# Performance work log

Hardware: AMD Instinct MI355X
Metric: run time of the kernel (lower is better)

The kernel has to match this reference:

```python
import jax, jax.numpy as jnp
import numpy as np

B, S, D_MODEL, H = 4, 2048, 1024, 16
D_K = D_MODEL // H


def setup_inputs() -> dict:
    key = jax.random.key(0)
    kx, kq, kk, kv, ko = jax.random.split(key, 5)
    scale = 1.0 / np.sqrt(D_MODEL)
    return {
        "x": jax.random.normal(kx, (B, S, D_MODEL), dtype=jnp.float32),
        "W_q": jax.random.normal(kq, (D_MODEL, D_MODEL), dtype=jnp.float32) * scale,
        "W_k": jax.random.normal(kk, (D_MODEL, D_MODEL), dtype=jnp.float32) * scale,
        "W_v": jax.random.normal(kv, (D_MODEL, D_MODEL), dtype=jnp.float32) * scale,
        "W_out": jax.random.normal(ko, (D_MODEL, D_MODEL), dtype=jnp.float32) * scale,
    }


def reference(x, W_q, W_k, W_v, W_out):
    # nn.Linear(bias=False): y = x @ W.T; weights stored as (out, in).
    Bx, Sx, D = x.shape
    q = (x @ W_q.T).reshape(Bx, Sx, H, D_K).transpose(0, 2, 1, 3)  # (B,H,S,d_k)
    k = (x @ W_k.T).reshape(Bx, Sx, H, D_K).transpose(0, 2, 1, 3)
    v = (x @ W_v.T).reshape(Bx, Sx, H, D_K).transpose(0, 2, 1, 3)
    scores = jnp.einsum("bhsd,bhtd->bhst", q, k) / jnp.sqrt(jnp.float32(D_K))
    attn = jax.nn.softmax(scores, axis=-1)
    out = jnp.einsum("bhst,bhtd->bhsd", attn, v)  # (B,H,S,d_k)
    out = out.transpose(0, 2, 1, 3).reshape(Bx, Sx, D)  # combine heads
    return out @ W_out.T
```

## Files before the change

### kernel.cpp

```cpp
#include <hip/hip_runtime.h>

#define BATCH 4
#define SEQ 2048
#define DM 1024
#define NH 16
#define DK 64

typedef unsigned short u16;
typedef unsigned int u32;
typedef __attribute__((ext_vector_type(8))) short bfrag;
typedef __attribute__((ext_vector_type(4))) float ffrag;

__device__ inline u16 f2bf(float f) {
  union { float f; u32 u; } v; v.f = f;
  u32 u = v.u;
  return (u16)((u + 0x7FFFu + ((u >> 16) & 1u)) >> 16);
}
__device__ inline float bf2f(u16 u) {
  union { u32 u; float f; } v; v.u = ((u32)u) << 16;
  return v.f;
}
__device__ inline ffrag MFMA(bfrag a, bfrag b, ffrag c) {
  return __builtin_amdgcn_mfma_f32_16x16x32_bf16(a, b, c, 0, 0, 0);
}

__device__ __forceinline__ void g2l16(const u16* g, u16* l) {
  __builtin_amdgcn_global_load_lds(
      (const __attribute__((address_space(1))) u16*)g,
      (__attribute__((address_space(3))) u16*)l, 16, 0, 0);
}

__global__ __launch_bounds__(256) void cvt_all(
    const float* __restrict__ x,
    const float* __restrict__ a, const float* __restrict__ b,
    const float* __restrict__ c, const float* __restrict__ d,
    u16* __restrict__ ox,
    u16* __restrict__ oa, u16* __restrict__ ob,
    u16* __restrict__ oc, u16* __restrict__ od) {
  int blk = blockIdx.x;
  const float* in;
  u16* out;
  int i;
  if (blk < 8192) {
    in = x; out = ox; i = blk * 256 + threadIdx.x;
  } else {
    int wb = blk - 8192;
    int which = wb >> 10;
    in = which == 0 ? a : which == 1 ? b : which == 2 ? c : d;
    out = which == 0 ? oa : which == 1 ? ob : which == 2 ? oc : od;
    i = (wb & 1023) * 256 + threadIdx.x;
  }
  float4 v = ((const float4*)in)[i];
  union { u16 u[4]; uint2 dd; } o;
  o.u[0] = f2bf(v.x); o.u[1] = f2bf(v.y); o.u[2] = f2bf(v.z); o.u[3] = f2bf(v.w);
  ((uint2*)out)[i] = o.dd;
}

__global__ __launch_bounds__(256) void gemm_qkv(
    const u16* __restrict__ xb,
    const u16* __restrict__ Wq, const u16* __restrict__ Wk,
    const u16* __restrict__ Wv,
    u16* __restrict__ Qb, u16* __restrict__ Ksw, u16* __restrict__ Vsw) {
  const int bid = blockIdx.x;
  const int xcd = bid & 7, s8 = bid >> 3;
  const int ym = (xcd << 3) | (s8 & 7);
  const int xn = (s8 >> 3) & 7;
  const int z = s8 >> 6;
  const u16* Bm = z == 0 ? Wq : z == 1 ? Wk : Wv;

  const int K = DM;
  const int bm = ym * 128, bn = xn * 128;
  __shared__ __align__(16) u16 As[128 * 64];
  __shared__ __align__(16) u16 Bs[128 * 64];
  const int tid = threadIdx.x;
  const int lane = tid & 63;
  const int w = tid >> 6;
  const int wr = w >> 1, wc = w & 1;
  const int l15 = lane & 15, quad = lane >> 4;
  const int srow = tid >> 3;
  const int scol = (((tid & 7) ^ (srow & 7)) * 8);

  ffrag acc[4][4] = {};

  for (int k0 = 0; k0 < K; k0 += 64) {
    __syncthreads();
#pragma unroll
    for (int c = 0; c < 4; c++) {
      g2l16(&xb[(size_t)(bm + c * 32 + srow) * K + k0 + scol], &As[c * 2048 + tid * 8]);
      g2l16(&Bm[(size_t)(bn + c * 32 + srow) * K + k0 + scol], &Bs[c * 2048 + tid * 8]);
    }
    __syncthreads();
#pragma unroll
    for (int kk = 0; kk < 2; kk++) {
      bfrag af[4], bf[4];
      if (z == 2) {
#pragma unroll
        for (int i = 0; i < 4; i++)
          af[i] = *(const bfrag*)(&As[(wr * 64 + i * 16 + l15) * 64 +
                                      ((kk * 4 + quad) ^ (l15 & 7)) * 8]);
#pragma unroll
        for (int j = 0; j < 4; j++)
          bf[j] = *(const bfrag*)(&Bs[(wc * 64 + j * 16 + l15) * 64 +
                                      ((kk * 4 + quad) ^ (l15 & 7)) * 8]);
      } else {
#pragma unroll
        for (int i = 0; i < 4; i++)
          af[i] = *(const bfrag*)(&Bs[(wr * 64 + i * 16 + l15) * 64 +
                                      ((kk * 4 + quad) ^ (l15 & 7)) * 8]);
#pragma unroll
        for (int j = 0; j < 4; j++)
          bf[j] = *(const bfrag*)(&As[(wc * 64 + j * 16 + l15) * 64 +
                                      ((kk * 4 + quad) ^ (l15 & 7)) * 8]);
      }
#pragma unroll
      for (int i = 0; i < 4; i++)
#pragma unroll
        for (int j = 0; j < 4; j++)
          acc[i][j] = MFMA(af[i], bf[j], acc[i][j]);
    }
  }

  if (z == 0) {
#pragma unroll
    for (int i = 0; i < 4; i++)
#pragma unroll
      for (int j = 0; j < 4; j++) {
        int mo = bn + wr * 64 + i * 16 + quad * 4;
        int nt = bm + wc * 64 + j * 16 + l15;
        int b = nt >> 11, s = nt & 2047;
        int h = mo >> 6, d = mo & 63;
        union { u16 u[4]; uint2 dd; } o;
#pragma unroll
        for (int r = 0; r < 4; r++) o.u[r] = f2bf(acc[i][j][r]);
        *(uint2*)(&Qb[(((size_t)(b * NH + h)) * SEQ + s) * DK + d]) = o.dd;
      }
  } else if (z == 1) {
#pragma unroll
    for (int i = 0; i < 4; i++)
#pragma unroll
      for (int j = 0; j < 4; j++) {
        int mo = bn + wr * 64 + i * 16 + quad * 4;
        int nt = bm + wc * 64 + j * 16 + l15;
        int b = nt >> 11, s = nt & 2047;
        int h = mo >> 6;
        size_t hb = (size_t)(b * NH + h) * (SEQ * DK);
        size_t off = hb + (size_t)(s >> 6) * 4096 +
            (size_t)((j * 2 + (i >> 1)) * 64 +
                     ((i * 2 + (quad >> 1)) & 3) * 16 + l15) * 8 +
            (quad & 1) * 4;
        union { u16 u[4]; uint2 dd; } o;
#pragma unroll
        for (int r = 0; r < 4; r++) o.u[r] = f2bf(acc[i][j][r]);
        *(uint2*)(&Ksw[off]) = o.dd;
      }
  } else {
#pragma unroll
    for (int i = 0; i < 4; i++)
#pragma unroll
      for (int j = 0; j < 4; j++) {
        int mt = bm + wr * 64 + i * 16 + quad * 4;
        int no = bn + wc * 64 + j * 16 + l15;
        int b = mt >> 11, s = mt & 2047;
        int h = no >> 6;
        size_t hb = (size_t)(b * NH + h) * (SEQ * DK);
        size_t off = hb + (size_t)(s >> 6) * 4096 +
            (size_t)((j * 2 + (i >> 1)) * 64 + quad * 16 + l15) * 8 +
            (i & 1) * 4;
        union { u16 u[4]; uint2 dd; } o;
#pragma unroll
        for (int r = 0; r < 4; r++) o.u[r] = f2bf(acc[i][j][r]);
        *(uint2*)(&Vsw[off]) = o.dd;
      }
  }
}

__global__ __launch_bounds__(256) void gemm_out(
    const u16* __restrict__ Ab, const u16* __restrict__ Wo, float* __restrict__ C) {
  const int K = DM, N = DM;
  const int bid = blockIdx.x;
  const int xcd = bid & 7, s8 = bid >> 3;
  const int ym = (xcd << 3) | (s8 & 7);
  const int xn = s8 >> 3;
  const int bm = ym * 128, bn = xn * 128;
  __shared__ __align__(16) u16 As[128 * 64];
  __shared__ __align__(16) u16 Bs[128 * 64];
  const int tid = threadIdx.x;
  const int lane = tid & 63;
  const int w = tid >> 6;
  const int wr = w >> 1, wc = w & 1;
  const int l15 = lane & 15, quad = lane >> 4;
  const int srow = tid >> 3;
  const int scol = (((tid & 7) ^ (srow & 7)) * 8);

  ffrag acc[4][4] = {};

  for (int k0 = 0; k0 < K; k0 += 64) {
    __syncthreads();
#pragma unroll
    for (int c = 0; c < 4; c++) {
      g2l16(&Ab[(size_t)(bm + c * 32 + srow) * K + k0 + scol], &As[c * 2048 + tid * 8]);
      g2l16(&Wo[(size_t)(bn + c * 32 + srow) * K + k0 + scol], &Bs[c * 2048 + tid * 8]);
    }
    __syncthreads();
#pragma unroll
    for (int kk = 0; kk < 2; kk++) {
      bfrag af[4], bf[4];
#pragma unroll
      for (int i = 0; i < 4; i++)
        af[i] = *(const bfrag*)(&Bs[(wr * 64 + i * 16 + l15) * 64 +
                                    ((kk * 4 + quad) ^ (l15 & 7)) * 8]);
#pragma unroll
      for (int j = 0; j < 4; j++)
        bf[j] = *(const bfrag*)(&As[(wc * 64 + j * 16 + l15) * 64 +
                                    ((kk * 4 + quad) ^ (l15 & 7)) * 8]);
#pragma unroll
      for (int i = 0; i < 4; i++)
#pragma unroll
        for (int j = 0; j < 4; j++)
          acc[i][j] = MFMA(af[i], bf[j], acc[i][j]);
    }
  }

#pragma unroll
  for (int i = 0; i < 4; i++)
#pragma unroll
    for (int j = 0; j < 4; j++) {
      int no = bn + wr * 64 + i * 16 + quad * 4;
      int mt = bm + wc * 64 + j * 16 + l15;
      *(ffrag*)(&C[(size_t)mt * N + no]) = acc[i][j];
    }
}

__global__ __launch_bounds__(256) void attn(
    const u16* __restrict__ Qb, const u16* __restrict__ Ksw,
    const u16* __restrict__ Vsw, u16* __restrict__ Ab) {
  const int bh = blockIdx.x;
  const int b = bh >> 4, h = bh & 15;
  const int qbase = blockIdx.y * 128;
  const int tid = threadIdx.x;
  const int w = tid >> 6, lane = tid & 63;
  const int l15 = lane & 15, quad = lane >> 4;

  __shared__ __align__(16) u16 Kt[2][4096];
  __shared__ __align__(16) u16 Vt[2][4096];

  const size_t hbase = (size_t)bh * SEQ * DK;

  const float qscale = 0.125f * 1.4426950408889634f;
  bfrag q[2][2];
#pragma unroll
  for (int i = 0; i < 2; i++)
#pragma unroll
    for (int kk = 0; kk < 2; kk++) {
      bfrag t = *(const bfrag*)(&Qb[hbase +
          (size_t)(qbase + w * 32 + i * 16 + l15) * DK + kk * 32 + quad * 8]);
#pragma unroll
      for (int e = 0; e < 8; e++)
        q[i][kk][e] = (short)f2bf(bf2f((u16)t[e]) * qscale);
    }

  ffrag O[4][2] = {};
  float lsum[2] = {0.f, 0.f};

  {
    const u16* ks = &Ksw[hbase];
    const u16* vs = &Vsw[hbase];
    g2l16(&ks[tid * 8], &Kt[0][tid * 8]);
    g2l16(&ks[2048 + tid * 8], &Kt[0][2048 + tid * 8]);
    g2l16(&vs[tid * 8], &Vt[0][tid * 8]);
    g2l16(&vs[2048 + tid * 8], &Vt[0][2048 + tid * 8]);
  }

  for (int t = 0; t < SEQ / 64; t++) {
    const int buf = t & 1;
    __syncthreads();
    if (t + 1 < SEQ / 64) {
      const u16* ks = &Ksw[hbase + (size_t)(t + 1) * 4096];
      const u16* vs = &Vsw[hbase + (size_t)(t + 1) * 4096];
      g2l16(&ks[tid * 8], &Kt[buf ^ 1][tid * 8]);
      g2l16(&ks[2048 + tid * 8], &Kt[buf ^ 1][2048 + tid * 8]);
      g2l16(&vs[tid * 8], &Vt[buf ^ 1][tid * 8]);
      g2l16(&vs[2048 + tid * 8], &Vt[buf ^ 1][2048 + tid * 8]);
    }

    __builtin_amdgcn_s_setprio(1);
    u32 pb[4][2][2];
#pragma unroll
    for (int j = 0; j < 4; j++) {
      bfrag k0f = *(const bfrag*)(&Kt[buf][((j * 2 + 0) * 64 + lane) * 8]);
      bfrag k1f = *(const bfrag*)(&Kt[buf][((j * 2 + 1) * 64 + lane) * 8]);
#pragma unroll
      for (int i = 0; i < 2; i++) {
        ffrag z = {};
        z = MFMA(k0f, q[i][0], z);
        z = MFMA(k1f, q[i][1], z);
        u32 u[4]; float ts = 0.f;
#pragma unroll
        for (int r = 0; r < 4; r++) {
          float p = __builtin_amdgcn_exp2f(z[r]);
          u[r] = __float_as_uint(p);
          ts += __uint_as_float(u[r] & 0xffff0000u);
        }
        lsum[i] += ts;
        pb[j][i][0] = __builtin_amdgcn_perm(u[1], u[0], 0x07060302u);
        pb[j][i][1] = __builtin_amdgcn_perm(u[3], u[2], 0x07060302u);
      }
    }

#pragma unroll
    for (int wnd = 0; wnd < 2; wnd++) {
      union { u32 d[4]; bfrag v; } px0, px1;
      px0.d[0] = pb[2 * wnd][0][0];     px0.d[1] = pb[2 * wnd][0][1];
      px0.d[2] = pb[2 * wnd + 1][0][0]; px0.d[3] = pb[2 * wnd + 1][0][1];
      px1.d[0] = pb[2 * wnd][1][0];     px1.d[1] = pb[2 * wnd][1][1];
      px1.d[2] = pb[2 * wnd + 1][1][0]; px1.d[3] = pb[2 * wnd + 1][1][1];
#pragma unroll
      for (int db = 0; db < 4; db++) {
        bfrag vf = *(const bfrag*)(&Vt[buf][((db * 2 + wnd) * 64 + lane) * 8]);
        O[db][0] = MFMA(vf, px0.v, O[db][0]);
        O[db][1] = MFMA(vf, px1.v, O[db][1]);
      }
    }
    __builtin_amdgcn_s_setprio(0);
  }

  float rl[2];
#pragma unroll
  for (int i = 0; i < 2; i++) {
    float s = lsum[i];
    s += __shfl_xor(s, 16);
    s += __shfl_xor(s, 32);
    rl[i] = 1.0f / s;
  }

  const size_t obase = ((size_t)b * SEQ) * DM + (size_t)h * DK;
#pragma unroll
  for (int db = 0; db < 4; db++)
#pragma unroll
    for (int i = 0; i < 2; i++) {
      int s = qbase + w * 32 + i * 16 + l15;
      union { u16 u[4]; uint2 d; } o;
#pragma unroll
      for (int r = 0; r < 4; r++) o.u[r] = f2bf(O[db][i][r] * rl[i]);
      *(uint2*)(&Ab[obase + (size_t)s * DM + db * 16 + quad * 4]) = o.d;
    }
}

extern "C" void kernel_launch(void* const* d_in, const int* in_sizes, int n_in,
                              void* d_out, int out_size, void* d_ws, size_t ws_size,
                              hipStream_t stream) {
  const float* x  = (const float*)d_in[0];
  const float* Wq = (const float*)d_in[1];
  const float* Wk = (const float*)d_in[2];
  const float* Wv = (const float*)d_in[3];
  const float* Wo = (const float*)d_in[4];
  float* out = (float*)d_out;

  char* ws = (char*)d_ws;
  u16* xb  = (u16*)(ws + 0);
  u16* Wqb = (u16*)(ws + 16777216);
  u16* Wkb = (u16*)(ws + 18874368);
  u16* Wvb = (u16*)(ws + 20971520);
  u16* Wob = (u16*)(ws + 23068672);
  u16* Qb  = (u16*)(ws + 25165824);
  u16* Ksw = (u16*)(ws + 41943040);
  u16* Vsw = (u16*)(ws + 58720256);
  u16* Ab  = (u16*)(ws + 75497472);
  const size_t NEED = 92274688;
  if (ws_size < NEED) return;

  cvt_all<<<12288, 256, 0, stream>>>(x, Wq, Wk, Wv, Wo, xb, Wqb, Wkb, Wvb, Wob);

  gemm_qkv<<<1536, 256, 0, stream>>>(xb, Wqb, Wkb, Wvb, Qb, Ksw, Vsw);

  dim3 gat(BATCH * NH, SEQ / 128);
  attn<<<gat, 256, 0, stream>>>(Qb, Ksw, Vsw, Ab);

  gemm_out<<<512, 256, 0, stream>>>(Ab, Wob, out);
}
```

Baseline: 268.5 us.

## Double-buffer LDS tiles in QKV and output GEMMs with K-tile 32

```diff
diff --git a/kernel.cpp b/kernel.cpp
--- a/kernel.cpp
+++ b/kernel.cpp
@@ -70,54 +70,55 @@
 
   const int K = DM;
   const int bm = ym * 128, bn = xn * 128;
-  __shared__ __align__(16) u16 As[128 * 64];
-  __shared__ __align__(16) u16 Bs[128 * 64];
+  __shared__ __align__(16) u16 As[2][128 * 32];
+  __shared__ __align__(16) u16 Bs[2][128 * 32];
   const int tid = threadIdx.x;
   const int lane = tid & 63;
   const int w = tid >> 6;
   const int wr = w >> 1, wc = w & 1;
   const int l15 = lane & 15, quad = lane >> 4;
-  const int srow = tid >> 3;
-  const int scol = (((tid & 7) ^ (srow & 7)) * 8);
+  const int srow = tid >> 2;
+  const int scol = (((tid & 3) ^ ((tid >> 3) & 3)) * 8);
+  const int sq = (quad ^ ((l15 >> 1) & 3)) * 8;
 
   ffrag acc[4][4] = {};
 
-  for (int k0 = 0; k0 < K; k0 += 64) {
+  g2l16(&xb[(size_t)(bm + srow) * K + scol], &As[0][tid * 8]);
+  g2l16(&xb[(size_t)(bm + 64 + srow) * K + scol], &As[0][(tid + 256) * 8]);
+  g2l16(&Bm[(size_t)(bn + srow) * K + scol], &Bs[0][tid * 8]);
+  g2l16(&Bm[(size_t)(bn + 64 + srow) * K + scol], &Bs[0][(tid + 256) * 8]);
+
+  for (int kt = 0; kt < K / 32; ++kt) {
+    const int buf = kt & 1;
     __syncthreads();
-#pragma unroll
-    for (int c = 0; c < 4; c++) {
-      g2l16(&xb[(size_t)(bm + c * 32 + srow) * K + k0 + scol], &As[c * 2048 + tid * 8]);
-      g2l16(&Bm[(size_t)(bn + c * 32 + srow) * K + k0 + scol], &Bs[c * 2048 + tid * 8]);
-    }
-    __syncthreads();
-#pragma unroll
-    for (int kk = 0; kk < 2; kk++) {
-      bfrag af[4], bf[4];
-      if (z == 2) {
-#pragma unroll
-        for (int i = 0; i < 4; i++)
-          af[i] = *(const bfrag*)(&As[(wr * 64 + i * 16 + l15) * 64 +
-                                      ((kk * 4 + quad) ^ (l15 & 7)) * 8]);
-#pragma unroll
-        for (int j = 0; j < 4; j++)
-          bf[j] = *(const bfrag*)(&Bs[(wc * 64 + j * 16 + l15) * 64 +
-                                      ((kk * 4 + quad) ^ (l15 & 7)) * 8]);
-      } else {
-#pragma unroll
-        for (int i = 0; i < 4; i++)
-          af[i] = *(const bfrag*)(&Bs[(wr * 64 + i * 16 + l15) * 64 +
-                                      ((kk * 4 + quad) ^ (l15 & 7)) * 8]);
-#pragma unroll
-        for (int j = 0; j < 4; j++)
-          bf[j] = *(const bfrag*)(&As[(wc * 64 + j * 16 + l15) * 64 +
-                                      ((kk * 4 + quad) ^ (l15 & 7)) * 8]);
-      }
+    if (kt + 1 < K / 32) {
+      const int k1 = (kt + 1) * 32;
+      g2l16(&xb[(size_t)(bm + srow) * K + k1 + scol], &As[buf ^ 1][tid * 8]);
+      g2l16(&xb[(size_t)(bm + 64 + srow) * K + k1 + scol], &As[buf ^ 1][(tid + 256) * 8]);
+      g2l16(&Bm[(size_t)(bn + srow) * K + k1 + scol], &Bs[buf ^ 1][tid * 8]);
+      g2l16(&Bm[(size_t)(bn + 64 + srow) * K + k1 + scol], &Bs[buf ^ 1][(tid + 256) * 8]);
+    }
+    bfrag af[4], bf[4];
+    if (z == 2) {
 #pragma unroll
       for (int i = 0; i < 4; i++)
-#pragma unroll
-        for (int j = 0; j < 4; j++)
-          acc[i][j] = MFMA(af[i], bf[j], acc[i][j]);
-    }
+        af[i] = *(const bfrag*)(&As[buf][(wr * 64 + i * 16 + l15) * 32 + sq]);
+#pragma unroll
+      for (int j = 0; j < 4; j++)
+        bf[j] = *(const bfrag*)(&Bs[buf][(wc * 64 + j * 16 + l15) * 32 + sq]);
+    } else {
+#pragma unroll
+      for (int i = 0; i < 4; i++)
+        af[i] = *(const bfrag*)(&Bs[buf][(wr * 64 + i * 16 + l15) * 32 + sq]);
+#pragma unroll
+      for (int j = 0; j < 4; j++)
+        bf[j] = *(const bfrag*)(&As[buf][(wc * 64 + j * 16 + l15) * 32 + sq]);
+    }
+#pragma unroll
+    for (int i = 0; i < 4; i++)
+#pragma unroll
+      for (int j = 0; j < 4; j++)
+        acc[i][j] = MFMA(af[i], bf[j], acc[i][j]);
   }
 
   if (z == 0) {
@@ -139,8 +140,8 @@
     for (int i = 0; i < 4; i++)
 #pragma unroll
       for (int j = 0; j < 4; j++) {
+        int nt = bm + wc * 64 + j * 16 + l15;
         int mo = bn + wr * 64 + i * 16 + quad * 4;
-        int nt = bm + wc * 64 + j * 16 + l15;
         int b = nt >> 11, s = nt & 2047;
         int h = mo >> 6;
         size_t hb = (size_t)(b * NH + h) * (SEQ * DK);
@@ -182,43 +183,46 @@
   const int ym = (xcd << 3) | (s8 & 7);
   const int xn = s8 >> 3;
   const int bm = ym * 128, bn = xn * 128;
-  __shared__ __align__(16) u16 As[128 * 64];
-  __shared__ __align__(16) u16 Bs[128 * 64];
+  __shared__ __align__(16) u16 As[2][128 * 32];
+  __shared__ __align__(16) u16 Bs[2][128 * 32];
   const int tid = threadIdx.x;
   const int lane = tid & 63;
   const int w = tid >> 6;
   const int wr = w >> 1, wc = w & 1;
   const int l15 = lane & 15, quad = lane >> 4;
-  const int srow = tid >> 3;
-  const int scol = (((tid & 7) ^ (srow & 7)) * 8);
+  const int srow = tid >> 2;
+  const int scol = (((tid & 3) ^ ((tid >> 3) & 3)) * 8);
+  const int sq = (quad ^ ((l15 >> 1) & 3)) * 8;
 
   ffrag acc[4][4] = {};
 
-  for (int k0 = 0; k0 < K; k0 += 64) {
+  g2l16(&Ab[(size_t)(bm + srow) * K + scol], &As[0][tid * 8]);
+  g2l16(&Ab[(size_t)(bm + 64 + srow) * K + scol], &As[0][(tid + 256) * 8]);
+  g2l16(&Wo[(size_t)(bn + srow) * K + scol], &Bs[0][tid * 8]);
+  g2l16(&Wo[(size_t)(bn + 64 + srow) * K + scol], &Bs[0][(tid + 256) * 8]);
+
+  for (int kt = 0; kt < K / 32; ++kt) {
+    const int buf = kt & 1;
     __syncthreads();
-#pragma unroll
-    for (int c = 0; c < 4; c++) {
-      g2l16(&Ab[(size_t)(bm + c * 32 + srow) * K + k0 + scol], &As[c * 2048 + tid * 8]);
-      g2l16(&Wo[(size_t)(bn + c * 32 + srow) * K + k0 + scol], &Bs[c * 2048 + tid * 8]);
-    }
-    __syncthreads();
-#pragma unroll
-    for (int kk = 0; kk < 2; kk++) {
-      bfrag af[4], bf[4];
-#pragma unroll
-      for (int i = 0; i < 4; i++)
-        af[i] = *(const bfrag*)(&Bs[(wr * 64 + i * 16 + l15) * 64 +
-                                    ((kk * 4 + quad) ^ (l15 & 7)) * 8]);
+    if (kt + 1 < K / 32) {
+      const int k1 = (kt + 1) * 32;
+      g2l16(&Ab[(size_t)(bm + srow) * K + k1 + scol], &As[buf ^ 1][tid * 8]);
+      g2l16(&Ab[(size_t)(bm + 64 + srow) * K + k1 + scol], &As[buf ^ 1][(tid + 256) * 8]);
+      g2l16(&Wo[(size_t)(bn + srow) * K + k1 + scol], &Bs[buf ^ 1][tid * 8]);
+      g2l16(&Wo[(size_t)(bn + 64 + srow) * K + k1 + scol], &Bs[buf ^ 1][(tid + 256) * 8]);
+    }
+    bfrag af[4], bf[4];
+#pragma unroll
+    for (int i = 0; i < 4; i++)
+      af[i] = *(const bfrag*)(&Bs[buf][(wr * 64 + i * 16 + l15) * 32 + sq]);
+#pragma unroll
+    for (int j = 0; j < 4; j++)
+      bf[j] = *(const bfrag*)(&As[buf][(wc * 64 + j * 16 + l15) * 32 + sq]);
+#pragma unroll
+    for (int i = 0; i < 4; i++)
 #pragma unroll
       for (int j = 0; j < 4; j++)
-        bf[j] = *(const bfrag*)(&As[(wc * 64 + j * 16 + l15) * 64 +
-                                    ((kk * 4 + quad) ^ (l15 & 7)) * 8]);
-#pragma unroll
-      for (int i = 0; i < 4; i++)
-#pragma unroll
-        for (int j = 0; j < 4; j++)
-          acc[i][j] = MFMA(af[i], bf[j], acc[i][j]);
-    }
+        acc[i][j] = MFMA(af[i], bf[j], acc[i][j]);
   }
 
 #pragma unroll
```

After: 282.6 us. 5.2% more time.

## Double attention query tile to 256 rows and fold Q scale into QKV GEMM

Applied to the files above, without the earlier changes.

```diff
diff --git a/kernel.cpp b/kernel.cpp
--- a/kernel.cpp
+++ b/kernel.cpp
@@ -121,6 +121,7 @@
   }
 
   if (z == 0) {
+    const float qscale = 0.125f * 1.4426950408889634f;
 #pragma unroll
     for (int i = 0; i < 4; i++)
 #pragma unroll
@@ -131,7 +132,7 @@
         int h = mo >> 6, d = mo & 63;
         union { u16 u[4]; uint2 dd; } o;
 #pragma unroll
-        for (int r = 0; r < 4; r++) o.u[r] = f2bf(acc[i][j][r]);
+        for (int r = 0; r < 4; r++) o.u[r] = f2bf(acc[i][j][r] * qscale);
         *(uint2*)(&Qb[(((size_t)(b * NH + h)) * SEQ + s) * DK + d]) = o.dd;
       }
   } else if (z == 1) {
@@ -139,8 +140,8 @@
     for (int i = 0; i < 4; i++)
 #pragma unroll
       for (int j = 0; j < 4; j++) {
+        int nt = bm + wc * 64 + j * 16 + l15;
         int mo = bn + wr * 64 + i * 16 + quad * 4;
-        int nt = bm + wc * 64 + j * 16 + l15;
         int b = nt >> 11, s = nt & 2047;
         int h = mo >> 6;
         size_t hb = (size_t)(b * NH + h) * (SEQ * DK);
@@ -231,56 +232,44 @@
     }
 }
 
-__global__ __launch_bounds__(256) void attn(
+__global__ __launch_bounds__(512) void attn(
     const u16* __restrict__ Qb, const u16* __restrict__ Ksw,
     const u16* __restrict__ Vsw, u16* __restrict__ Ab) {
   const int bh = blockIdx.x;
   const int b = bh >> 4, h = bh & 15;
-  const int qbase = blockIdx.y * 128;
+  const int qbase = blockIdx.y * 256;
   const int tid = threadIdx.x;
   const int w = tid >> 6, lane = tid & 63;
   const int l15 = lane & 15, quad = lane >> 4;
+  const int qoff = (w >> 2) * 128 + (w & 3) * 32;
 
   __shared__ __align__(16) u16 Kt[2][4096];
   __shared__ __align__(16) u16 Vt[2][4096];
 
   const size_t hbase = (size_t)bh * SEQ * DK;
 
-  const float qscale = 0.125f * 1.4426950408889634f;
   bfrag q[2][2];
 #pragma unroll
   for (int i = 0; i < 2; i++)
 #pragma unroll
-    for (int kk = 0; kk < 2; kk++) {
-      bfrag t = *(const bfrag*)(&Qb[hbase +
-          (size_t)(qbase + w * 32 + i * 16 + l15) * DK + kk * 32 + quad * 8]);
-#pragma unroll
-      for (int e = 0; e < 8; e++)
-        q[i][kk][e] = (short)f2bf(bf2f((u16)t[e]) * qscale);
-    }
+    for (int kk = 0; kk < 2; kk++)
+      q[i][kk] = *(const bfrag*)(&Qb[hbase +
+          (size_t)(qbase + qoff + i * 16 + l15) * DK + kk * 32 + quad * 8]);
 
   ffrag O[4][2] = {};
   float lsum[2] = {0.f, 0.f};
 
   {
-    const u16* ks = &Ksw[hbase];
-    const u16* vs = &Vsw[hbase];
-    g2l16(&ks[tid * 8], &Kt[0][tid * 8]);
-    g2l16(&ks[2048 + tid * 8], &Kt[0][2048 + tid * 8]);
-    g2l16(&vs[tid * 8], &Vt[0][tid * 8]);
-    g2l16(&vs[2048 + tid * 8], &Vt[0][2048 + tid * 8]);
+    g2l16(&Ksw[hbase + tid * 8], &Kt[0][tid * 8]);
+    g2l16(&Vsw[hbase + tid * 8], &Vt[0][tid * 8]);
   }
 
   for (int t = 0; t < SEQ / 64; t++) {
     const int buf = t & 1;
     __syncthreads();
     if (t + 1 < SEQ / 64) {
-      const u16* ks = &Ksw[hbase + (size_t)(t + 1) * 4096];
-      const u16* vs = &Vsw[hbase + (size_t)(t + 1) * 4096];
-      g2l16(&ks[tid * 8], &Kt[buf ^ 1][tid * 8]);
-      g2l16(&ks[2048 + tid * 8], &Kt[buf ^ 1][2048 + tid * 8]);
-      g2l16(&vs[tid * 8], &Vt[buf ^ 1][tid * 8]);
-      g2l16(&vs[2048 + tid * 8], &Vt[buf ^ 1][2048 + tid * 8]);
+      g2l16(&Ksw[hbase + (size_t)(t + 1) * 4096 + tid * 8], &Kt[buf ^ 1][tid * 8]);
+      g2l16(&Vsw[hbase + (size_t)(t + 1) * 4096 + tid * 8], &Vt[buf ^ 1][tid * 8]);
     }
 
     __builtin_amdgcn_s_setprio(1);
@@ -338,7 +327,7 @@
   for (int db = 0; db < 4; db++)
 #pragma unroll
     for (int i = 0; i < 2; i++) {
-      int s = qbase + w * 32 + i * 16 + l15;
+      int s = qbase + qoff + i * 16 + l15;
       union { u16 u[4]; uint2 d; } o;
 #pragma unroll
       for (int r = 0; r < 4; r++) o.u[r] = f2bf(O[db][i][r] * rl[i]);
@@ -373,8 +362,8 @@
 
   gemm_qkv<<<1536, 256, 0, stream>>>(xb, Wqb, Wkb, Wvb, Qb, Ksw, Vsw);
 
-  dim3 gat(BATCH * NH, SEQ / 128);
-  attn<<<gat, 256, 0, stream>>>(Qb, Ksw, Vsw, Ab);
+  dim3 gat(BATCH * NH, SEQ / 256);
+  attn<<<gat, 512, 0, stream>>>(Qb, Ksw, Vsw, Ab);
 
   gemm_out<<<512, 256, 0, stream>>>(Ab, Wob, out);
 }
```

Measured after the change: 291.7 us. 8.6% more time.
